# Optimization experiments

Hardware: AMD Instinct MI355X
Metric: run time of the kernel (lower is better)

Reference implementation:

```python
import jax, jax.numpy as jnp
import numpy as np

B, N, C = 2, 2048, 768
H = 16
D = C // H  # head_dim = 48
SCALE = 1.0 / float(np.sqrt(D))


def setup_inputs() -> dict:
    key = jax.random.key(0)
    ks = jax.random.split(key, 5)
    x = jax.random.normal(ks[0], (B, N, C), dtype=jnp.float32)
    # torch nn.Linear weights are [out, in]; apply as x @ W.T
    qkv_w = jax.random.normal(ks[1], (3 * C, C), dtype=jnp.float32) * 0.02
    qkv_b = jax.random.normal(ks[2], (3 * C,), dtype=jnp.float32) * 0.02
    proj_w = jax.random.normal(ks[3], (C, C), dtype=jnp.float32) * 0.02
    proj_b = jax.random.normal(ks[4], (C,), dtype=jnp.float32) * 0.02
    return {"x": x, "qkv_w": qkv_w, "qkv_b": qkv_b, "proj_w": proj_w, "proj_b": proj_b}


def reference(x, qkv_w, qkv_b, proj_w, proj_b):
    # qkv: (B, N, 3C) -> (3, B, H, N, D)
    qkv = x @ qkv_w.T + qkv_b
    qkv = qkv.reshape(B, N, 3, H, D).transpose(2, 0, 3, 1, 4)
    q, k, v = qkv[0], qkv[1], qkv[2]
    # manual attention: full (B, H, N, N) score matrix, as in the original
    attn = jnp.einsum('bhqd,bhkd->bhqk', q, k) * SCALE
    attn = jax.nn.softmax(attn, axis=-1)
    # attn_drop with p=0.0 (eval / deterministic) is identity
    y = jnp.einsum('bhqk,bhkd->bhqd', attn, v)
    y = y.transpose(0, 2, 1, 3).reshape(B, N, C)
    return y @ proj_w.T + proj_b
```

## Files before the change

kernel.cpp:

```cpp
#include <hip/hip_runtime.h>

typedef short v8s __attribute__((ext_vector_type(8)));
typedef short v4s __attribute__((ext_vector_type(4)));
typedef float v4f __attribute__((ext_vector_type(4)));
typedef unsigned short u16;

#define NSEQ 2048
#define CDIM 768
#define NH   16
#define DH   48
#define DP   64
#define MROWS 4096
#define N3C  2304
#define BH   32

#if __has_builtin(__builtin_amdgcn_exp2f)
#define EXP2(x) __builtin_amdgcn_exp2f(x)
#else
#define EXP2(x) exp2f(x)
#endif
#if __has_builtin(__builtin_amdgcn_rcpf)
#define RCP(x) __builtin_amdgcn_rcpf(x)
#else
#define RCP(x) (1.0f/(x))
#endif

__device__ __forceinline__ u16 f2bf(float f){
  unsigned u = __float_as_uint(f);
  u += 0x7FFFu + ((u>>16)&1u);
  return (u16)(u>>16);
}

__device__ __forceinline__ void load_lds16(const u16* g, u16* l){
  __builtin_amdgcn_global_load_lds((const __attribute__((address_space(1))) void*)g,
                                   (__attribute__((address_space(3))) void*)l, 16, 0, 0);
}

#define XN8  (MROWS*CDIM/8)
#define WN8  (N3C*CDIM/8)
#define PN8  (CDIM*CDIM/8)
#define CONVB ((XN8+WN8+PN8)/256)
__global__ __launch_bounds__(256) void prep(const float* __restrict__ x, const float* __restrict__ w,
                                            const float* __restrict__ pw, u16* __restrict__ dst,
                                            u16* __restrict__ q, u16* __restrict__ k, u16* __restrict__ v){
  int bid = blockIdx.x;
  if (bid < CONVB){
    int i = bid*256 + threadIdx.x;
    const float* src;
    if (i < XN8)            src = x  + (size_t)i*8;
    else if (i < XN8+WN8)   src = w  + (size_t)(i - XN8)*8;
    else                    src = pw + (size_t)(i - XN8 - WN8)*8;
    v4f f0 = ((const v4f*)src)[0];
    v4f f1 = ((const v4f*)src)[1];
    v8s o;
#pragma unroll
    for (int j = 0; j < 4; j++) ((u16*)&o)[j]   = f2bf(f0[j]);
#pragma unroll
    for (int j = 0; j < 4; j++) ((u16*)&o)[4+j] = f2bf(f1[j]);
    ((v8s*)dst)[i] = o;
  } else {
    int idx = (bid - CONVB)*256 + threadIdx.x;
    v8s z = (v8s){0,0,0,0,0,0,0,0};
    int r = idx >> 1, half = idx & 1;
    *(v8s*)(q + (size_t)r*DP + DH + half*8) = z;
    *(v8s*)(k + (size_t)r*DP + DH + half*8) = z;
    int bh = idx >> 12, i = idx & 4095;
    int row = i >> 8, off = i & 255;
    const short one = (short)0x3F80;
    v8s val = (row == 0) ? (v8s){one,one,one,one,one,one,one,one} : z;
    *(v8s*)(v + ((size_t)(bh*DP + DH + row))*NSEQ + off*8) = val;
  }
}

__global__ __launch_bounds__(256) void qkv_gemm(const u16* __restrict__ x, const u16* __restrict__ w,
                                                const float* __restrict__ bias,
                                                u16* __restrict__ q, u16* __restrict__ k, u16* __restrict__ v){
  __shared__ __align__(16) u16 As[128*32];
  __shared__ __align__(16) u16 Bs[128*32];
  const int wave = threadIdx.x >> 6;
  const int lane = threadIdx.x & 63;
  const int l15  = lane & 15;
  const int quad = lane >> 4;
  const int wm = wave & 1, wn = wave >> 1;
  const int m0 = blockIdx.x*128, n0 = blockIdx.y*128;

  const int srow = lane >> 2;
  const int sg   = (lane & 3) ^ ((lane >> 3) & 3);
  const int sgoff = sg*8;

  v4f acc[4][4];
#pragma unroll
  for (int i = 0; i < 4; i++)
#pragma unroll
    for (int j = 0; j < 4; j++) acc[i][j] = (v4f){0.f,0.f,0.f,0.f};

  const int sig = (l15 >> 1) & 3;

  for (int kt = 0; kt < CDIM/32; kt++){
    const int k0 = kt*32;
    __syncthreads();
#pragma unroll
    for (int j = 0; j < 2; j++){
      int c = wave*2 + j;
      int r = c*16 + srow;
      load_lds16(x + (size_t)(m0 + r)*CDIM + k0 + sgoff, &As[c*512]);
      load_lds16(w + (size_t)(n0 + r)*CDIM + k0 + sgoff, &Bs[c*512]);
    }
    __syncthreads();

    v8s af[4], bf[4];
#pragma unroll
    for (int t = 0; t < 4; t++){
      int ra = wm*64 + t*16 + l15;
      af[t] = *(const v8s*)(&As[ra*32 + ((quad ^ sig)<<3)]);
      int rb = wn*64 + t*16 + l15;
      bf[t] = *(const v8s*)(&Bs[rb*32 + ((quad ^ sig)<<3)]);
    }
#pragma unroll
    for (int ti = 0; ti < 4; ti++)
#pragma unroll
      for (int tj = 0; tj < 4; tj++)
        acc[ti][tj] = __builtin_amdgcn_mfma_f32_16x16x32_bf16(af[ti], bf[tj], acc[ti][tj], 0, 0, 0);
  }

  const float QS = 0.2082540589f;
#pragma unroll
  for (int tj = 0; tj < 4; tj++){
    const int c = n0 + wn*64 + tj*16 + l15;
    const float bv = bias[c];
    const int t = c / CDIM;
    const int rem = c - t*CDIM;
    const int h = rem / DH;
    const int d = rem - h*DH;
#pragma unroll
    for (int ti = 0; ti < 4; ti++){
#pragma unroll
      for (int r = 0; r < 4; r++){
        int m = m0 + wm*64 + ti*16 + quad*4 + r;
        int b_ = m >> 11;
        int n  = m & (NSEQ-1);
        float val = acc[ti][tj][r] + bv;
        if (t == 0) val *= QS;
        u16 o  = f2bf(val);
        int bhn = b_*NH + h;
        if (t == 0)      q[((size_t)bhn*NSEQ + n)*DP + d] = o;
        else if (t == 1) k[((size_t)bhn*NSEQ + n)*DP + d] = o;
        else             v[((size_t)bhn*DP + d)*NSEQ + n] = o;
      }
    }
  }
}

__global__ __launch_bounds__(256) void attn(const u16* __restrict__ q, const u16* __restrict__ k,
                                            const u16* __restrict__ v,
                                            float* __restrict__ oacc, float* __restrict__ lacc){
  __shared__ __align__(16) u16 Kl[64*64];
  __shared__ __align__(16) u16 Vl[64*64];
  __shared__ __align__(16) u16 Pl[4][16*64];
  const int bh = blockIdx.x;
  const int qt = blockIdx.y;
  const int sp = blockIdx.z;
  const int wave = threadIdx.x >> 6;
  const int lane = threadIdx.x & 63;
  const int l15  = lane & 15;
  const int quad = lane >> 4;
  const u16* qb = q + (size_t)bh*NSEQ*DP;
  const u16* kb = k + (size_t)bh*NSEQ*DP;
  const u16* vb = v + (size_t)bh*DP*NSEQ;
  const int qm = qt*64 + wave*16;

  v8s qf[2];
#pragma unroll
  for (int ks = 0; ks < 2; ks++)
    qf[ks] = *(const v8s*)(qb + (size_t)(qm + l15)*DP + ks*32 + quad*8);

  v4f o[4];
#pragma unroll
  for (int i = 0; i < 4; i++) o[i] = (v4f){0.f,0.f,0.f,0.f};

  int pwoff[4][4];
#pragma unroll
  for (int nt = 0; nt < 4; nt++)
#pragma unroll
    for (int r = 0; r < 4; r++){
      int row = quad*4 + r;
      int col = nt*16 + l15;
      pwoff[nt][r] = row*64 + ((((col>>3) ^ (row&7))<<3) | (col&7));
    }

  for (int kt = sp*16; kt < sp*16 + 16; kt++){
    __syncthreads();
    {
      const int t = threadIdx.x;
#pragma unroll
      for (int p = 0; p < 2; p++){
        int ci  = t + p*256;
        int row = ci >> 3;
        int off = ci & 7;
        v8s kd = *(const v8s*)(kb + (size_t)(kt*64 + row)*DP + off*8);
        *(v8s*)(&Kl[row*64 + ((off ^ (row&7))<<3)]) = kd;
        v8s vd = *(const v8s*)(vb + (size_t)row*NSEQ + kt*64 + off*8);
        *(v8s*)(&Vl[row*64 + ((off ^ (row&7))<<3)]) = vd;
      }
    }
    __syncthreads();

    v4f s[4];
#pragma unroll
    for (int nt = 0; nt < 4; nt++){
      s[nt] = (v4f){0.f,0.f,0.f,0.f};
#pragma unroll
      for (int ks = 0; ks < 2; ks++){
        int rrow = nt*16 + l15;
        v8s bf = *(const v8s*)(&Kl[rrow*64 + (((ks*4+quad) ^ (rrow&7))<<3)]);
        s[nt] = __builtin_amdgcn_mfma_f32_16x16x32_bf16(qf[ks], bf, s[nt], 0, 0, 0);
      }
    }

#pragma unroll
    for (int nt = 0; nt < 4; nt++)
#pragma unroll
      for (int r = 0; r < 4; r++)
        Pl[wave][pwoff[nt][r]] = f2bf(EXP2(s[nt][r]));

    v8s pa[2];
#pragma unroll
    for (int ks = 0; ks < 2; ks++){
      int ga = ks*4 + quad;
      pa[ks] = *(const v8s*)(&Pl[wave][l15*64 + ((ga ^ (l15&7))<<3)]);
    }
#pragma unroll
    for (int dt = 0; dt < 4; dt++){
#pragma unroll
      for (int ks = 0; ks < 2; ks++){
        int row = dt*16 + l15;
        v8s vf = *(const v8s*)(&Vl[row*64 + (((ks*4+quad) ^ (row&7))<<3)]);
        o[dt] = __builtin_amdgcn_mfma_f32_16x16x32_bf16(pa[ks], vf, o[dt], 0, 0, 0);
      }
    }
  }

  const int b_ = bh / NH, h = bh % NH;
  float* oa = oacc + (size_t)sp*MROWS*CDIM;
  float* la = lacc + (size_t)sp*MROWS*NH;
#pragma unroll
  for (int r = 0; r < 4; r++){
    int rowg = b_*NSEQ + qm + quad*4 + r;
#pragma unroll
    for (int dt = 0; dt < 3; dt++)
      oa[(size_t)rowg*CDIM + h*DH + dt*16 + l15] = o[dt][r];
    if (l15 == 0) la[rowg*NH + h] = o[3][r];
  }
}

__global__ __launch_bounds__(256) void finalize(const float* __restrict__ oacc,
                                                const float* __restrict__ lacc,
                                                u16* __restrict__ y){
  int i = blockIdx.x*256 + threadIdx.x;
  int rowg = i / 192, c4 = i - rowg*192;
  int c = c4*4, h = c / DH;
  float l = lacc[rowg*NH + h] + lacc[MROWS*NH + rowg*NH + h];
  float inv = RCP(l);
  v4f a = *(const v4f*)(oacc + (size_t)rowg*CDIM + c);
  v4f b = *(const v4f*)(oacc + (size_t)MROWS*CDIM + (size_t)rowg*CDIM + c);
  v4s o4;
#pragma unroll
  for (int j = 0; j < 4; j++) o4[j] = (short)f2bf((a[j] + b[j])*inv);
  *(v4s*)(y + (size_t)rowg*CDIM + c) = o4;
}

__global__ __launch_bounds__(256) void proj_gemm(const u16* __restrict__ y, const u16* __restrict__ w,
                                                 const float* __restrict__ bias, float* __restrict__ out){
  __shared__ __align__(16) u16 As[64*32];
  __shared__ __align__(16) u16 Bs[128*32];
  const int wave = threadIdx.x >> 6;
  const int lane = threadIdx.x & 63;
  const int l15  = lane & 15;
  const int quad = lane >> 4;
  const int wm = wave & 1, wn = wave >> 1;
  const int m0 = blockIdx.x*64, n0 = blockIdx.y*128;

  const int srow = lane >> 2;
  const int sg   = (lane & 3) ^ ((lane >> 3) & 3);
  const int sgoff = sg*8;

  v4f acc[2][4];
#pragma unroll
  for (int i = 0; i < 2; i++)
#pragma unroll
    for (int j = 0; j < 4; j++) acc[i][j] = (v4f){0.f,0.f,0.f,0.f};

  const int sig = (l15 >> 1) & 3;

  for (int kt = 0; kt < CDIM/32; kt++){
    const int k0 = kt*32;
    __syncthreads();
    {
      int rA = wave*16 + srow;
      load_lds16(y + (size_t)(m0 + rA)*CDIM + k0 + sgoff, &As[wave*512]);
#pragma unroll
      for (int j = 0; j < 2; j++){
        int c = wave*2 + j;
        int rB = c*16 + srow;
        load_lds16(w + (size_t)(n0 + rB)*CDIM + k0 + sgoff, &Bs[c*512]);
      }
    }
    __syncthreads();

    v8s af[2], bf[4];
#pragma unroll
    for (int t = 0; t < 2; t++){
      int ra = wm*32 + t*16 + l15;
      af[t] = *(const v8s*)(&As[ra*32 + ((quad ^ sig)<<3)]);
    }
#pragma unroll
    for (int t = 0; t < 4; t++){
      int rb = wn*64 + t*16 + l15;
      bf[t] = *(const v8s*)(&Bs[rb*32 + ((quad ^ sig)<<3)]);
    }
#pragma unroll
    for (int ti = 0; ti < 2; ti++)
#pragma unroll
      for (int tj = 0; tj < 4; tj++)
        acc[ti][tj] = __builtin_amdgcn_mfma_f32_16x16x32_bf16(af[ti], bf[tj], acc[ti][tj], 0, 0, 0);
  }

#pragma unroll
  for (int tj = 0; tj < 4; tj++){
    const int c = n0 + wn*64 + tj*16 + l15;
    const float bv = bias[c];
#pragma unroll
    for (int ti = 0; ti < 2; ti++){
#pragma unroll
      for (int r = 0; r < 4; r++){
        int m = m0 + wm*32 + ti*16 + quad*4 + r;
        out[(size_t)m*CDIM + c] = acc[ti][tj][r] + bv;
      }
    }
  }
}

extern "C" void kernel_launch(void* const* d_in, const int* in_sizes, int n_in,
                              void* d_out, int out_size, void* d_ws, size_t ws_size,
                              hipStream_t stream){
  const float* x      = (const float*)d_in[0];
  const float* qkv_w  = (const float*)d_in[1];
  const float* qkv_b  = (const float*)d_in[2];
  const float* proj_w = (const float*)d_in[3];
  const float* proj_b = (const float*)d_in[4];
  float* out = (float*)d_out;

  u16* xb  = (u16*)d_ws;
  u16* wb  = xb  + (size_t)MROWS*CDIM;
  u16* pwb = wb  + (size_t)N3C*CDIM;
  u16* q   = pwb + (size_t)CDIM*CDIM;
  u16* k   = q + (size_t)BH*NSEQ*DP;
  u16* v   = k + (size_t)BH*NSEQ*DP;
  float* oacc = (float*)(v + (size_t)BH*NSEQ*DP);
  float* lacc = oacc + (size_t)2*MROWS*CDIM;
  u16* y = xb;

  prep<<<dim3(CONVB + 512), dim3(256), 0, stream>>>(x, qkv_w, proj_w, xb, q, k, v);
  qkv_gemm<<<dim3(MROWS/128, N3C/128), dim3(256), 0, stream>>>(xb, wb, qkv_b, q, k, v);
  attn<<<dim3(BH, NSEQ/64, 2), dim3(256), 0, stream>>>(q, k, v, oacc, lacc);
  finalize<<<dim3(MROWS*192/256), dim3(256), 0, stream>>>(oacc, lacc, y);
  proj_gemm<<<dim3(MROWS/64, CDIM/128), dim3(256), 0, stream>>>(y, pwb, proj_b, out);
}
```

Before: 185.0 us.

## Process two query subtiles per wave and load K/V directly into LDS

The attention kernel now gives each wave 32 query rows as two 16-row subtiles, and each block 128 queries. Every K/V tile staged in LDS is therefore reused by twice as many queries, and the grid is halved. K and V tiles are loaded with global_load_lds instead of staging through registers. The score MFMA has its operands swapped so exponentiated probabilities can be written to LDS as packed bf16 pairs. The row-sum is now computed by an MFMA against a register constant of ones, so the padded V rows and their initialisation in prep are no longer needed. The cost is higher register pressure from doubled accumulators, and fewer blocks for occupancy.

Result: faster. 174.4 us (-5.7%).

```diff
diff --git a/kernel.cpp b/kernel.cpp
--- a/kernel.cpp
+++ b/kernel.cpp
@@ -3,6 +3,7 @@
 typedef short v8s __attribute__((ext_vector_type(8)));
 typedef short v4s __attribute__((ext_vector_type(4)));
 typedef float v4f __attribute__((ext_vector_type(4)));
+typedef unsigned uint2v __attribute__((ext_vector_type(2)));
 typedef unsigned short u16;
 
 #define NSEQ 2048
@@ -29,6 +30,12 @@
   unsigned u = __float_as_uint(f);
   u += 0x7FFFu + ((u>>16)&1u);
   return (u16)(u>>16);
+}
+__device__ __forceinline__ unsigned pkbf(float a, float b){
+  unsigned x = __float_as_uint(a), y = __float_as_uint(b);
+  x += 0x7FFFu + ((x>>16)&1u);
+  y += 0x7FFFu + ((y>>16)&1u);
+  return (x>>16) | (y & 0xFFFF0000u);
 }
 
 __device__ __forceinline__ void load_lds16(const u16* g, u16* l){
@@ -64,11 +71,6 @@
     int r = idx >> 1, half = idx & 1;
     *(v8s*)(q + (size_t)r*DP + DH + half*8) = z;
     *(v8s*)(k + (size_t)r*DP + DH + half*8) = z;
-    int bh = idx >> 12, i = idx & 4095;
-    int row = i >> 8, off = i & 255;
-    const short one = (short)0x3F80;
-    v8s val = (row == 0) ? (v8s){one,one,one,one,one,one,one,one} : z;
-    *(v8s*)(v + ((size_t)(bh*DP + DH + row))*NSEQ + off*8) = val;
   }
 }
 
@@ -155,8 +157,8 @@
                                             const u16* __restrict__ v,
                                             float* __restrict__ oacc, float* __restrict__ lacc){
   __shared__ __align__(16) u16 Kl[64*64];
-  __shared__ __align__(16) u16 Vl[64*64];
-  __shared__ __align__(16) u16 Pl[4][16*64];
+  __shared__ __align__(16) u16 Vl[48*64];
+  __shared__ __align__(16) u16 Pl[4*2*1024];
   const int bh = blockIdx.x;
   const int qt = blockIdx.y;
   const int sp = blockIdx.z;
@@ -164,79 +166,97 @@
   const int lane = threadIdx.x & 63;
   const int l15  = lane & 15;
   const int quad = lane >> 4;
+  const int lo3  = l15 & 7;
   const u16* qb = q + (size_t)bh*NSEQ*DP;
   const u16* kb = k + (size_t)bh*NSEQ*DP;
   const u16* vb = v + (size_t)bh*DP*NSEQ;
-  const int qm = qt*64 + wave*16;
-
-  v8s qf[2];
-#pragma unroll
-  for (int ks = 0; ks < 2; ks++)
-    qf[ks] = *(const v8s*)(qb + (size_t)(qm + l15)*DP + ks*32 + quad*8);
-
-  v4f o[4];
-#pragma unroll
-  for (int i = 0; i < 4; i++) o[i] = (v4f){0.f,0.f,0.f,0.f};
-
-  int pwoff[4][4];
-#pragma unroll
-  for (int nt = 0; nt < 4; nt++)
-#pragma unroll
-    for (int r = 0; r < 4; r++){
-      int row = quad*4 + r;
-      int col = nt*16 + l15;
-      pwoff[nt][r] = row*64 + ((((col>>3) ^ (row&7))<<3) | (col&7));
-    }
+  const int qm = qt*128 + wave*32;
+
+  v8s qf[2][2];
+#pragma unroll
+  for (int si = 0; si < 2; si++)
+#pragma unroll
+    for (int ks = 0; ks < 2; ks++)
+      qf[si][ks] = *(const v8s*)(qb + (size_t)(qm + si*16 + l15)*DP + ks*32 + quad*8);
+
+  const short one = (short)0x3F80;
+  const v8s vones = (l15 == 0) ? (v8s){one,one,one,one,one,one,one,one}
+                               : (v8s){0,0,0,0,0,0,0,0};
+
+  v4f o[2][4];
+#pragma unroll
+  for (int si = 0; si < 2; si++)
+#pragma unroll
+    for (int i = 0; i < 4; i++) o[si][i] = (v4f){0.f,0.f,0.f,0.f};
+
+  const int sr  = lane >> 3;
+  const int soff = ((lane & 7) ^ (sr & 7)) * 8;
+  u16* Plw = Pl + wave*2048;
 
   for (int kt = sp*16; kt < sp*16 + 16; kt++){
     __syncthreads();
     {
-      const int t = threadIdx.x;
 #pragma unroll
       for (int p = 0; p < 2; p++){
-        int ci  = t + p*256;
-        int row = ci >> 3;
-        int off = ci & 7;
-        v8s kd = *(const v8s*)(kb + (size_t)(kt*64 + row)*DP + off*8);
-        *(v8s*)(&Kl[row*64 + ((off ^ (row&7))<<3)]) = kd;
-        v8s vd = *(const v8s*)(vb + (size_t)row*NSEQ + kt*64 + off*8);
-        *(v8s*)(&Vl[row*64 + ((off ^ (row&7))<<3)]) = vd;
-      }
-    }
-    __syncthreads();
-
-    v4f s[4];
-#pragma unroll
-    for (int nt = 0; nt < 4; nt++){
-      s[nt] = (v4f){0.f,0.f,0.f,0.f};
+        int row = p*32 + wave*8 + sr;
+        load_lds16(kb + ((size_t)(kt*64 + row))*DP + soff, &Kl[(p*32 + wave*8)*64]);
+      }
+      {
+        int row = wave*8 + sr;
+        load_lds16(vb + (size_t)row*NSEQ + kt*64 + soff, &Vl[(wave*8)*64]);
+      }
+      if (wave < 2){
+        int row = 32 + wave*8 + sr;
+        load_lds16(vb + (size_t)row*NSEQ + kt*64 + soff, &Vl[(32 + wave*8)*64]);
+      }
+    }
+    __syncthreads();
+
+#pragma unroll
+    for (int si = 0; si < 2; si++){
+      v4f s[4];
+#pragma unroll
+      for (int nt = 0; nt < 4; nt++){
+        s[nt] = (v4f){0.f,0.f,0.f,0.f};
+#pragma unroll
+        for (int ks = 0; ks < 2; ks++){
+          int rrow = nt*16 + l15;
+          v8s kf = *(const v8s*)(&Kl[rrow*64 + (((ks*4+quad) ^ lo3)<<3)]);
+          s[nt] = __builtin_amdgcn_mfma_f32_16x16x32_bf16(kf, qf[si][ks], s[nt], 0, 0, 0);
+        }
+      }
+#pragma unroll
+      for (int nt = 0; nt < 4; nt++){
+        uint2v pw;
+        pw.x = pkbf(EXP2(s[nt][0]), EXP2(s[nt][1]));
+        pw.y = pkbf(EXP2(s[nt][2]), EXP2(s[nt][3]));
+        int g = nt*2 + (quad>>1);
+        *(uint2v*)(&Plw[si*1024 + l15*64 + ((g ^ lo3)<<3) + (quad&1)*4]) = pw;
+      }
+    }
+
+    v8s pa[2][2];
+#pragma unroll
+    for (int si = 0; si < 2; si++)
 #pragma unroll
       for (int ks = 0; ks < 2; ks++){
-        int rrow = nt*16 + l15;
-        v8s bf = *(const v8s*)(&Kl[rrow*64 + (((ks*4+quad) ^ (rrow&7))<<3)]);
-        s[nt] = __builtin_amdgcn_mfma_f32_16x16x32_bf16(qf[ks], bf, s[nt], 0, 0, 0);
-      }
-    }
-
-#pragma unroll
-    for (int nt = 0; nt < 4; nt++)
-#pragma unroll
-      for (int r = 0; r < 4; r++)
-        Pl[wave][pwoff[nt][r]] = f2bf(EXP2(s[nt][r]));
-
-    v8s pa[2];
-#pragma unroll
-    for (int ks = 0; ks < 2; ks++){
-      int ga = ks*4 + quad;
-      pa[ks] = *(const v8s*)(&Pl[wave][l15*64 + ((ga ^ (l15&7))<<3)]);
-    }
-#pragma unroll
-    for (int dt = 0; dt < 4; dt++){
+        int ga = ks*4 + quad;
+        pa[si][ks] = *(const v8s*)(&Plw[si*1024 + l15*64 + ((ga ^ lo3)<<3)]);
+      }
+#pragma unroll
+    for (int dt = 0; dt < 3; dt++){
 #pragma unroll
       for (int ks = 0; ks < 2; ks++){
         int row = dt*16 + l15;
-        v8s vf = *(const v8s*)(&Vl[row*64 + (((ks*4+quad) ^ (row&7))<<3)]);
-        o[dt] = __builtin_amdgcn_mfma_f32_16x16x32_bf16(pa[ks], vf, o[dt], 0, 0, 0);
-      }
+        v8s vf = *(const v8s*)(&Vl[row*64 + (((ks*4+quad) ^ lo3)<<3)]);
+        o[0][dt] = __builtin_amdgcn_mfma_f32_16x16x32_bf16(pa[0][ks], vf, o[0][dt], 0, 0, 0);
+        o[1][dt] = __builtin_amdgcn_mfma_f32_16x16x32_bf16(pa[1][ks], vf, o[1][dt], 0, 0, 0);
+      }
+    }
+#pragma unroll
+    for (int ks = 0; ks < 2; ks++){
+      o[0][3] = __builtin_amdgcn_mfma_f32_16x16x32_bf16(pa[0][ks], vones, o[0][3], 0, 0, 0);
+      o[1][3] = __builtin_amdgcn_mfma_f32_16x16x32_bf16(pa[1][ks], vones, o[1][3], 0, 0, 0);
     }
   }
 
@@ -244,12 +264,15 @@
   float* oa = oacc + (size_t)sp*MROWS*CDIM;
   float* la = lacc + (size_t)sp*MROWS*NH;
 #pragma unroll
-  for (int r = 0; r < 4; r++){
-    int rowg = b_*NSEQ + qm + quad*4 + r;
-#pragma unroll
-    for (int dt = 0; dt < 3; dt++)
-      oa[(size_t)rowg*CDIM + h*DH + dt*16 + l15] = o[dt][r];
-    if (l15 == 0) la[rowg*NH + h] = o[3][r];
+  for (int si = 0; si < 2; si++){
+#pragma unroll
+    for (int r = 0; r < 4; r++){
+      int rowg = b_*NSEQ + qm + si*16 + quad*4 + r;
+#pragma unroll
+      for (int dt = 0; dt < 3; dt++)
+        oa[(size_t)rowg*CDIM + h*DH + dt*16 + l15] = o[si][dt][r];
+      if (l15 == 0) la[rowg*NH + h] = o[si][3][r];
+    }
   }
 }
 
@@ -362,7 +385,7 @@
 
   prep<<<dim3(CONVB + 512), dim3(256), 0, stream>>>(x, qkv_w, proj_w, xb, q, k, v);
   qkv_gemm<<<dim3(MROWS/128, N3C/128), dim3(256), 0, stream>>>(xb, wb, qkv_b, q, k, v);
-  attn<<<dim3(BH, NSEQ/64, 2), dim3(256), 0, stream>>>(q, k, v, oacc, lacc);
+  attn<<<dim3(BH, NSEQ/128, 2), dim3(256), 0, stream>>>(q, k, v, oacc, lacc);
   finalize<<<dim3(MROWS*192/256), dim3(256), 0, stream>>>(oacc, lacc, y);
   proj_gemm<<<dim3(MROWS/64, CDIM/128), dim3(256), 0, stream>>>(y, pwb, proj_b, out);
 }
```
